# Performance work log

Measured on AMD Instinct MI355X. Metric: run time of the kernel, lower is better.

The kernel has to match this reference:

```python
import jax, jax.numpy as jnp
import numpy as np

B = 16384      # batch size
D = 512        # state_dim (= number of graph nodes)
HID = 512      # hidden_dim of main GCN blocks
EH = 32        # hidden dim of ENSO GCN blocks
K = 2          # fourier_modes
OMEGA = 2.0 * np.pi / 12.0


def setup_inputs() -> dict:
    ks = jax.random.split(jax.random.key(0), 20)
    def w(k, shape, scale=0.05):
        return (jax.random.normal(k, shape) * scale).astype(jnp.float32)
    inp = {
        "x": jax.random.normal(ks[0], (B, D), dtype=jnp.float32),
        "t": jax.random.uniform(ks[1], (1,), dtype=jnp.float32) * 12.0,
        "fourier_coeffs": w(ks[2], (D, D, 2 * K + 1), 0.1),
        # quadratic_graph: GCN(D->HID) -> ReLU -> GCN(HID->D)
        "quad_W1": w(ks[3], (D, HID)), "quad_b1": jnp.zeros((HID,), jnp.float32),
        "quad_W2": w(ks[4], (HID, D)), "quad_b2": jnp.zeros((D,), jnp.float32),
        # cubic_graph
        "cubic_W1": w(ks[5], (D, HID)), "cubic_b1": jnp.zeros((HID,), jnp.float32),
        "cubic_W2": w(ks[6], (HID, D)), "cubic_b2": jnp.zeros((D,), jnp.float32),
        # enso_T_graph: GCN(5->32) -> ReLU -> GCN(32->1)
        "ensoT_W1": w(ks[7], (5, EH)), "ensoT_b1": jnp.zeros((EH,), jnp.float32),
        "ensoT_W2": w(ks[8], (EH, 1)), "ensoT_b2": jnp.zeros((1,), jnp.float32),
        # enso_H_graph
        "ensoH_W1": w(ks[9], (5, EH)), "ensoH_b1": jnp.zeros((EH,), jnp.float32),
        "ensoH_W2": w(ks[10], (EH, 1)), "ensoH_b2": jnp.zeros((1,), jnp.float32),
    }
    return inp


def _gcn2(feat, W1, b1, W2, b2):
    # Fully-connected graph + self-loops => normalized adjacency P = (1/N) 11^T.
    # All node rows are identical (x expanded over nodes), so P @ X == X and every
    # node's output is identical: the 2-layer GCN collapses to two dense GEMMs.
    h = jax.nn.relu(feat @ W1 + b1)
    return h @ W2 + b2


def reference(x, t, fourier_coeffs,
              quad_W1, quad_b1, quad_W2, quad_b2,
              cubic_W1, cubic_b1, cubic_W2, cubic_b2,
              ensoT_W1, ensoT_b1, ensoT_W2, ensoT_b2,
              ensoH_W1, ensoH_b1, ensoH_W2, ensoH_b2):
    ts = t[0]
    # --- Seasonal linear operator L(t) = C0 + sum_k Ck^c cos(k w t) + Ck^s sin(k w t)
    L = fourier_coeffs[:, :, 0]
    for k in range(1, K + 1):
        L = L + fourier_coeffs[:, :, 2 * k - 1] * jnp.cos(k * OMEGA * ts)
        L = L + fourier_coeffs[:, :, 2 * k] * jnp.sin(k * OMEGA * ts)
    linear_term = jnp.einsum('ij,bj->bi', L, x)  # [B, D]

    # --- Graph nonlinear terms (per-node outputs identical; mean over feature dim)
    quad = _gcn2(x, quad_W1, quad_b1, quad_W2, quad_b2)        # [B, D]
    cubic = _gcn2(x, cubic_W1, cubic_b1, cubic_W2, cubic_b2)   # [B, D]
    # torch: out[node] identical for all nodes; .mean(dim=1) over features -> same
    # scalar replicated across the state dimension.
    quad_terms = jnp.broadcast_to(quad.mean(axis=1, keepdims=True), (x.shape[0], D))
    cubic_terms = jnp.broadcast_to(cubic.mean(axis=1, keepdims=True), (x.shape[0], D))
    nonlinear = quad_terms + cubic_terms

    # --- ENSO-specific physics (state_dim >= 2)
    T = x[:, 0:1]
    H = x[:, 1:2]
    fT = jnp.concatenate([T, H, T * T, T * H, T * T * T], axis=1)   # [B, 5]
    fH = jnp.concatenate([T, H, T * T, T * H, T * H * H], axis=1)   # [B, 5]
    cT = _gcn2(fT, ensoT_W1, ensoT_b1, ensoT_W2, ensoT_b2)  # [B, 1]
    cH = _gcn2(fH, ensoH_W1, ensoH_b1, ensoH_W2, ensoH_b2)  # [B, 1]
    pad = jnp.zeros((x.shape[0], D - 2), dtype=x.dtype)
    nonlinear = nonlinear + jnp.concatenate([cT, cH, pad], axis=1)

    return linear_term + nonlinear
```

## Files before the change

kernel.cpp:

```cpp
#include <hip/hip_runtime.h>


#define OMEGA_F 0.5235987755982988f

typedef __attribute__((ext_vector_type(8))) short short8;
typedef __attribute__((ext_vector_type(4))) float f32x4;

__device__ __forceinline__ unsigned short f2bf(float f) {
  union { float f; unsigned int u; } a;
  a.f = f;
  unsigned int u = a.u;
  return (unsigned short)((u + 0x7fffu + ((u >> 16) & 1u)) >> 16);
}

__device__ __forceinline__ void gload16(const void* g, void* l) {
  __builtin_amdgcn_global_load_lds(
      (const __attribute__((address_space(1))) unsigned int*)g,
      (__attribute__((address_space(3))) unsigned int*)l, 16, 0, 0);
}

__global__ void prep_conv(const float* __restrict__ fc, const float* __restrict__ qW1,
                          const float* __restrict__ cW1, const float* __restrict__ t,
                          const float* __restrict__ qW2, const float* __restrict__ cW2,
                          const float* __restrict__ qb2, const float* __restrict__ cb2,
                          const float4* __restrict__ x4, const float* __restrict__ x,
                          const float* __restrict__ tW1, const float* __restrict__ tb1,
                          const float* __restrict__ tW2, const float* __restrict__ tb2,
                          const float* __restrict__ hW1, const float* __restrict__ hb1,
                          const float* __restrict__ hW2, const float* __restrict__ hb2,
                          unsigned short* __restrict__ WT, uint2* __restrict__ xb,
                          float* __restrict__ qw2m, float* __restrict__ cw2m,
                          float* __restrict__ b2m, float* __restrict__ cT,
                          float* __restrict__ cH, float* __restrict__ rowadd) {
  int b = blockIdx.x, tdx = threadIdx.x;
  if (b < 3072) {
    int idx = b * 256 + tdx;
    int n = idx >> 9;
    int k = idx & 511;
    float v;
    if (n < 512) {
      float th = OMEGA_F * t[0];
      float s1, c1, s2, c2;
      sincosf(th, &s1, &c1);
      sincosf(2.0f * th, &s2, &c2);
      const float* p = fc + ((size_t)n * 512 + k) * 5;
      v = p[0] + p[1] * c1 + p[2] * s1 + p[3] * c2 + p[4] * s2;
    } else if (n < 1024) {
      v = qW1[(size_t)k * 512 + (n - 512)];
    } else {
      v = cW1[(size_t)k * 512 + (n - 1024)];
    }
    WT[idx] = f2bf(v);
  } else if (b < 3076) {
    int bb = b - 3072;
    const float* W = (bb < 2) ? qW2 : cW2;
    float* o = (bb < 2) ? qw2m : cw2m;
    int h = (bb & 1) * 256 + tdx;
    const float4* row = (const float4*)(W + (size_t)h * 512);
    float s = 0.f;
    for (int i = 0; i < 128; ++i) { float4 v = row[i]; s += (v.x + v.y) + (v.z + v.w); }
    o[h] = s * (1.0f / 512.0f);
  } else if (b == 3076) {
    __shared__ float sm[256];
    sm[tdx] = qb2[tdx] + qb2[tdx + 256];
    __syncthreads();
    for (int w = 128; w > 0; w >>= 1) { if (tdx < w) sm[tdx] += sm[tdx + w]; __syncthreads(); }
    if (tdx == 0) b2m[0] = sm[0] * (1.0f / 512.0f);
    __syncthreads();
    sm[tdx] = cb2[tdx] + cb2[tdx + 256];
    __syncthreads();
    for (int w = 128; w > 0; w >>= 1) { if (tdx < w) sm[tdx] += sm[tdx + w]; __syncthreads(); }
    if (tdx == 0) b2m[1] = sm[0] * (1.0f / 512.0f);
  } else if (b < 3077 + 8192) {
    int i = (b - 3077) * 256 + tdx;
    float4 v = x4[i];
    uint2 r;
    r.x = (unsigned)f2bf(v.x) | ((unsigned)f2bf(v.y) << 16);
    r.y = (unsigned)f2bf(v.z) | ((unsigned)f2bf(v.w) << 16);
    xb[i] = r;
  } else {
    int row = (b - 11269) * 256 + tdx;
    rowadd[row] = 0.f;
    float T = x[(size_t)row * 512];
    float H = x[(size_t)row * 512 + 1];
    float fT[5] = {T, H, T * T, T * H, T * T * T};
    float fH[5] = {T, H, T * T, T * H, T * H * H};
    float sT = tb2[0], sH = hb2[0];
#pragma unroll 4
    for (int e = 0; e < 32; ++e) {
      float a1 = tb1[e], a2 = hb1[e];
#pragma unroll
      for (int f = 0; f < 5; ++f) {
        a1 += fT[f] * tW1[f * 32 + e];
        a2 += fH[f] * hW1[f * 32 + e];
      }
      sT += fmaxf(a1, 0.f) * tW2[e];
      sH += fmaxf(a2, 0.f) * hW2[e];
    }
    cT[row] = sT;
    cH[row] = sH;
  }
}

#define GEMM_MAINLOOP(A_, Bt_, MB_, NB_)                                          \
  const int tid = threadIdx.x;                                                    \
  const int lane = tid & 63;                                                      \
  const int wave = tid >> 6;                                                      \
  const int wm = wave & 1;                                                        \
  const int wn = wave >> 1;                                                       \
  const int m_base = (MB_);                                                       \
  const int n_base = (NB_);                                                       \
  const int lrow = lane & 15;                                                     \
  const int l7 = lrow & 7;                                                        \
  const int kgrp = lane >> 4;                                                     \
  const int srow = lane >> 3;                                                     \
  const int sk = ((lane & 7) ^ srow) * 8;                                         \
  const unsigned short* gA0 = (A_) + (size_t)(m_base + wave * 8 + srow) * 512 + sk; \
  const unsigned short* gA1 = gA0 + 32 * 512;                                     \
  const unsigned short* gA2 = gA0 + 64 * 512;                                     \
  const unsigned short* gA3 = gA0 + 96 * 512;                                     \
  const unsigned short* gB0 = (Bt_) + (size_t)(n_base + wave * 8 + srow) * 512 + sk;\
  const unsigned short* gB1 = gB0 + 32 * 512;                                     \
  const unsigned short* gB2 = gB0 + 64 * 512;                                     \
  const unsigned short* gB3 = gB0 + 96 * 512;                                     \
  unsigned short* lA0 = As + wave * 512;                                          \
  unsigned short* lA1 = As + (4 + wave) * 512;                                    \
  unsigned short* lA2 = As + (8 + wave) * 512;                                    \
  unsigned short* lA3 = As + (12 + wave) * 512;                                   \
  unsigned short* lB0 = Bs + wave * 512;                                          \
  unsigned short* lB1 = Bs + (4 + wave) * 512;                                    \
  unsigned short* lB2 = Bs + (8 + wave) * 512;                                    \
  unsigned short* lB3 = Bs + (12 + wave) * 512;                                   \
  f32x4 acc[4][4];                                                                \
  _Pragma("unroll") for (int i = 0; i < 4; ++i)                                   \
      _Pragma("unroll") for (int j = 0; j < 4; ++j)                               \
          acc[i][j] = (f32x4){0.f, 0.f, 0.f, 0.f};                                \
  gload16(gA0, lA0); gload16(gA1, lA1); gload16(gA2, lA2); gload16(gA3, lA3);     \
  gload16(gB0, lB0); gload16(gB1, lB1); gload16(gB2, lB2); gload16(gB3, lB3);     \
  gA0 += 64; gA1 += 64; gA2 += 64; gA3 += 64;                                     \
  gB0 += 64; gB1 += 64; gB2 += 64; gB3 += 64;                                     \
  __syncthreads();                                                                \
  _Pragma("unroll") for (int kt = 0; kt < 8; ++kt) {                              \
    const int cur = (kt & 1) << 13;                                               \
    const int nxt = cur ^ 8192;                                                   \
    if (kt < 7) {                                                                 \
      gload16(gA0, lA0 + nxt); gload16(gA1, lA1 + nxt);                           \
      gload16(gA2, lA2 + nxt); gload16(gA3, lA3 + nxt);                           \
      gload16(gB0, lB0 + nxt); gload16(gB1, lB1 + nxt);                           \
      gload16(gB2, lB2 + nxt); gload16(gB3, lB3 + nxt);                           \
      gA0 += 64; gA1 += 64; gA2 += 64; gA3 += 64;                                 \
      gB0 += 64; gB1 += 64; gB2 += 64; gB3 += 64;                                 \
    }                                                                             \
    _Pragma("unroll") for (int h = 0; h < 2; ++h) {                               \
      short8 af[4], bfr[4];                                                       \
      const int ks = ((h * 4 + kgrp) ^ l7) * 8 + cur;                             \
      _Pragma("unroll") for (int i = 0; i < 4; ++i)                               \
          af[i] = *(const short8*)(&As[(wm * 64 + i * 16 + lrow) * 64 + ks]);     \
      _Pragma("unroll") for (int j = 0; j < 4; ++j)                               \
          bfr[j] = *(const short8*)(&Bs[(wn * 64 + j * 16 + lrow) * 64 + ks]);    \
      _Pragma("unroll") for (int i = 0; i < 4; ++i)                               \
          _Pragma("unroll") for (int j = 0; j < 4; ++j)                           \
              acc[i][j] = __builtin_amdgcn_mfma_f32_16x16x32_bf16(af[i], bfr[j],  \
                                                                  acc[i][j], 0, 0, 0); \
    }                                                                             \
    __syncthreads();                                                              \
  }

__global__ __launch_bounds__(256) void nl_gemm(
    const unsigned short* __restrict__ A,
    const unsigned short* __restrict__ Bt,
    const float* __restrict__ qb1, const float* __restrict__ cb1,
    const float* __restrict__ qw2m, const float* __restrict__ cw2m,
    float* __restrict__ rowadd) {
  __shared__ unsigned short As[2 * 128 * 64];
  __shared__ unsigned short Bs[2 * 128 * 64];
  float rs[4][4];
#pragma unroll
  for (int i = 0; i < 4; ++i)
#pragma unroll
    for (int r = 0; r < 4; ++r) rs[i][r] = 0.f;

  for (int t = 0; t < 2; ++t) {
    GEMM_MAINLOOP(A, Bt, blockIdx.x * 128, (blockIdx.y * 2 + t) * 128)
    const bool isq = (n_base < 512);
    const float* b1 = isq ? qb1 : cb1;
    const float* w2m = isq ? qw2m : cw2m;
    const int cb0 = (isq ? n_base : n_base - 512) + wn * 64 + lrow;
#pragma unroll
    for (int j = 0; j < 4; ++j) {
      int col = cb0 + j * 16;
      float bb = b1[col];
      float ww = w2m[col];
#pragma unroll
      for (int i = 0; i < 4; ++i)
#pragma unroll
        for (int r = 0; r < 4; ++r)
          rs[i][r] += fmaxf(acc[i][j][r] + bb, 0.f) * ww;
    }
  }

  const int lane_e = threadIdx.x & 63;
  const int wm_e = (threadIdx.x >> 6) & 1;
  const int rbase = blockIdx.x * 128 + wm_e * 64 + (lane_e >> 4) * 4;
#pragma unroll
  for (int i = 0; i < 4; ++i)
#pragma unroll
    for (int r = 0; r < 4; ++r) {
      float v = rs[i][r];
      v += __shfl_xor(v, 1, 64);
      v += __shfl_xor(v, 2, 64);
      v += __shfl_xor(v, 4, 64);
      v += __shfl_xor(v, 8, 64);
      if ((lane_e & 15) == 0) atomicAdd(&rowadd[rbase + i * 16 + r], v);
    }
}

__global__ __launch_bounds__(256) void lin_gemm(
    const unsigned short* __restrict__ A,
    const unsigned short* __restrict__ Bt,
    const float* __restrict__ rowadd, const float* __restrict__ b2m,
    const float* __restrict__ cT, const float* __restrict__ cH,
    float* __restrict__ out) {
  __shared__ unsigned short As[2 * 128 * 64];
  __shared__ unsigned short Bs[2 * 128 * 64];
  GEMM_MAINLOOP(A, Bt, blockIdx.x * 128, blockIdx.y * 128)
  const int rbase = m_base + wm * 64 + (lane >> 4) * 4;
  const float b2s = b2m[0] + b2m[1];
  float ra[4][4];
#pragma unroll
  for (int i = 0; i < 4; ++i)
#pragma unroll
    for (int r = 0; r < 4; ++r) ra[i][r] = rowadd[rbase + i * 16 + r] + b2s;
#pragma unroll
  for (int j = 0; j < 4; ++j) {
    int col = n_base + wn * 64 + j * 16 + lrow;
#pragma unroll
    for (int i = 0; i < 4; ++i)
#pragma unroll
      for (int r = 0; r < 4; ++r) {
        int row = rbase + i * 16 + r;
        float v = acc[i][j][r] + ra[i][r];
        if (col == 0) v += cT[row];
        if (col == 1) v += cH[row];
        out[(size_t)row * 512 + col] = v;
      }
  }
}

extern "C" void kernel_launch(void* const* d_in, const int* in_sizes, int n_in,
                              void* d_out, int out_size, void* d_ws, size_t ws_size,
                              hipStream_t stream) {
  const float* x   = (const float*)d_in[0];
  const float* t   = (const float*)d_in[1];
  const float* fc  = (const float*)d_in[2];
  const float* qW1 = (const float*)d_in[3];
  const float* qb1 = (const float*)d_in[4];
  const float* qW2 = (const float*)d_in[5];
  const float* qb2 = (const float*)d_in[6];
  const float* cW1 = (const float*)d_in[7];
  const float* cb1 = (const float*)d_in[8];
  const float* cW2 = (const float*)d_in[9];
  const float* cb2 = (const float*)d_in[10];
  const float* tW1 = (const float*)d_in[11];
  const float* tb1 = (const float*)d_in[12];
  const float* tW2 = (const float*)d_in[13];
  const float* tb2 = (const float*)d_in[14];
  const float* hW1 = (const float*)d_in[15];
  const float* hb1 = (const float*)d_in[16];
  const float* hW2 = (const float*)d_in[17];
  const float* hb2 = (const float*)d_in[18];
  float* out = (float*)d_out;

  char* ws = (char*)d_ws;
  unsigned short* WT = (unsigned short*)(ws);
  unsigned short* xb = (unsigned short*)(ws + 1572864);
  float* qw2m   = (float*)(ws + 18350080);
  float* cw2m   = (float*)(ws + 18352128);
  float* b2m    = (float*)(ws + 18354176);
  float* cT     = (float*)(ws + 18354432);
  float* cH     = (float*)(ws + 18419968);
  float* rowadd = (float*)(ws + 18485504);

  prep_conv<<<11333, 256, 0, stream>>>(fc, qW1, cW1, t, qW2, cW2, qb2, cb2,
                                       (const float4*)x, x,
                                       tW1, tb1, tW2, tb2, hW1, hb1, hW2, hb2,
                                       WT, (uint2*)xb, qw2m, cw2m, b2m, cT, cH,
                                       rowadd);
  nl_gemm<<<dim3(128, 4), 256, 0, stream>>>(xb, WT + (size_t)512 * 512,
                                            qb1, cb1, qw2m, cw2m, rowadd);
  lin_gemm<<<dim3(128, 4), 256, 0, stream>>>(xb, WT, rowadd, b2m, cT, cH, out);
}
```

Measured before the change: 180.9 us.

## Prefetch two K-stages ahead with partial vmcnt waits in GEMM mainloop

```diff
diff --git a/kernel.cpp b/kernel.cpp
--- a/kernel.cpp
+++ b/kernel.cpp
@@ -102,6 +102,14 @@
   }
 }
 
+#define GEMM_STAGE(off)                                                           \
+  gload16(gA0, lA0 + (off)); gload16(gA1, lA1 + (off));                           \
+  gload16(gA2, lA2 + (off)); gload16(gA3, lA3 + (off));                           \
+  gload16(gB0, lB0 + (off)); gload16(gB1, lB1 + (off));                           \
+  gload16(gB2, lB2 + (off)); gload16(gB3, lB3 + (off));                           \
+  gA0 += 64; gA1 += 64; gA2 += 64; gA3 += 64;                                     \
+  gB0 += 64; gB1 += 64; gB2 += 64; gB3 += 64;
+
 #define GEMM_MAINLOOP(A_, Bt_, MB_, NB_)                                          \
   const int tid = threadIdx.x;                                                    \
   const int lane = tid & 63;                                                      \
@@ -135,22 +143,14 @@
   _Pragma("unroll") for (int i = 0; i < 4; ++i)                                   \
       _Pragma("unroll") for (int j = 0; j < 4; ++j)                               \
           acc[i][j] = (f32x4){0.f, 0.f, 0.f, 0.f};                                \
-  gload16(gA0, lA0); gload16(gA1, lA1); gload16(gA2, lA2); gload16(gA3, lA3);     \
-  gload16(gB0, lB0); gload16(gB1, lB1); gload16(gB2, lB2); gload16(gB3, lB3);     \
-  gA0 += 64; gA1 += 64; gA2 += 64; gA3 += 64;                                     \
-  gB0 += 64; gB1 += 64; gB2 += 64; gB3 += 64;                                     \
-  __syncthreads();                                                                \
+  GEMM_STAGE(0)                                                                   \
+  GEMM_STAGE(8192)                                                                \
   _Pragma("unroll") for (int kt = 0; kt < 8; ++kt) {                              \
     const int cur = (kt & 1) << 13;                                               \
-    const int nxt = cur ^ 8192;                                                   \
-    if (kt < 7) {                                                                 \
-      gload16(gA0, lA0 + nxt); gload16(gA1, lA1 + nxt);                           \
-      gload16(gA2, lA2 + nxt); gload16(gA3, lA3 + nxt);                           \
-      gload16(gB0, lB0 + nxt); gload16(gB1, lB1 + nxt);                           \
-      gload16(gB2, lB2 + nxt); gload16(gB3, lB3 + nxt);                           \
-      gA0 += 64; gA1 += 64; gA2 += 64; gA3 += 64;                                 \
-      gB0 += 64; gB1 += 64; gB2 += 64; gB3 += 64;                                 \
-    }                                                                             \
+    if (kt == 7) { asm volatile("s_waitcnt vmcnt(0)" ::: "memory"); }             \
+    else         { asm volatile("s_waitcnt vmcnt(8)" ::: "memory"); }             \
+    __builtin_amdgcn_s_barrier();                                                 \
+    asm volatile("" ::: "memory");                                                \
     _Pragma("unroll") for (int h = 0; h < 2; ++h) {                               \
       short8 af[4], bfr[4];                                                       \
       const int ks = ((h * 4 + kgrp) ^ l7) * 8 + cur;                             \
@@ -163,7 +163,10 @@
               acc[i][j] = __builtin_amdgcn_mfma_f32_16x16x32_bf16(af[i], bfr[j],  \
                                                                   acc[i][j], 0, 0, 0); \
     }                                                                             \
-    __syncthreads();                                                              \
+    asm volatile("" ::: "memory");                                                \
+    __builtin_amdgcn_s_barrier();                                                 \
+    asm volatile("" ::: "memory");                                                \
+    if (kt < 6) { GEMM_STAGE(cur) }                                               \
   }
 
 __global__ __launch_bounds__(256) void nl_gemm(
```

Measured after the change: 177.0 us. 2.1% less time.
